# Optimization experiments

Measured on AMD Instinct MI355X. Metric: run time of the kernel, lower is better.

The kernel has to match this reference:

```python
import jax, jax.numpy as jnp
import numpy as np

B, L, D = 2, 2048, 2048
H, Hd = 16, 128


def _rotary_cos_sin(max_len, dim, base=10000.0):
    inv_freq = 1.0 / (base ** (np.arange(0, dim, 2, dtype=np.float32) / dim))
    t = np.arange(max_len, dtype=np.float32)
    freqs = np.outer(t, inv_freq)                      # [L, dim/2]
    emb = np.concatenate([freqs, freqs], axis=-1)      # [L, dim]
    cos = np.cos(emb)[None, None]                      # [1,1,L,dim]
    sin = np.sin(emb)[None, None]
    return jnp.asarray(cos), jnp.asarray(sin)


def setup_inputs() -> dict:
    key = jax.random.key(0)
    ks = jax.random.split(key, 5)
    hidden_states = jax.random.normal(ks[0], (B, L, D), dtype=jnp.float32)
    cos, sin = _rotary_cos_sin(L, Hd)
    s = 1.0 / np.sqrt(D)
    wq = jax.random.normal(ks[1], (H * Hd, D), dtype=jnp.float32) * s
    wk = jax.random.normal(ks[2], (H * Hd, D), dtype=jnp.float32) * s
    wv = jax.random.normal(ks[3], (H * Hd, D), dtype=jnp.float32) * s
    wo = jax.random.normal(ks[4], (D, H * Hd), dtype=jnp.float32) * s
    return {"hidden_states": hidden_states, "cos": cos, "sin": sin,
            "wq": wq, "wk": wk, "wv": wv, "wo": wo}


def _rotate_half(x):
    x1, x2 = jnp.split(x, 2, axis=-1)
    return jnp.concatenate([-x2, x1], axis=-1)


def reference(hidden_states, cos, sin, wq, wk, wv, wo):
    b, l, d = hidden_states.shape
    # QKV projections -> [B, H, L, Hd]
    q = (hidden_states @ wq.T).reshape(b, l, H, Hd).transpose(0, 2, 1, 3)
    k = (hidden_states @ wk.T).reshape(b, l, H, Hd).transpose(0, 2, 1, 3)
    v = (hidden_states @ wv.T).reshape(b, l, H, Hd).transpose(0, 2, 1, 3)
    c = cos[:, :, :l, :]
    s = sin[:, :, :l, :]
    q = q * c + _rotate_half(q) * s
    k = k * c + _rotate_half(k) * s
    # SDPA (non-causal, default scale = 1/sqrt(head_dim))
    scale = 1.0 / jnp.sqrt(jnp.asarray(Hd, dtype=q.dtype))
    scores = jnp.einsum('bhqd,bhkd->bhqk', q, k) * scale
    attn = jax.nn.softmax(scores, axis=-1)
    out = jnp.einsum('bhqk,bhkd->bhqd', attn, v)       # [B,H,L,Hd]
    out = out.transpose(0, 2, 1, 3).reshape(b, l, H * Hd)
    return out @ wo.T
```

## Files before the change

kernel.cpp:

```cpp
#include <hip/hip_runtime.h>

constexpr int Bb = 2;
constexpr int Ll = 2048;
constexpr int Dd = 2048;
constexpr int Hh = 16;
constexpr int Hd = 128;
constexpr int M  = Bb * Ll;

typedef __attribute__((ext_vector_type(8)))  short s16x8;
typedef __attribute__((ext_vector_type(4)))  float f32x4;
typedef __attribute__((ext_vector_type(16))) float f32x16;

__device__ __forceinline__ unsigned short f2bf(float f) {
    union { float f; unsigned u; } v; v.f = f;
    unsigned r = v.u + 0x7fffu + ((v.u >> 16) & 1u);
    return (unsigned short)(r >> 16);
}
__device__ __forceinline__ float bf2f(unsigned short b) {
    union { unsigned u; float f; } v; v.u = ((unsigned)b) << 16;
    return v.f;
}
__device__ __forceinline__ float fast_exp2(float x) {
#if __has_builtin(__builtin_amdgcn_exp2f)
    return __builtin_amdgcn_exp2f(x);
#else
    return exp2f(x);
#endif
}

__device__ __forceinline__ void gld16(const void* g, void* l) {
#if __has_builtin(__builtin_amdgcn_global_load_lds)
    __builtin_amdgcn_global_load_lds(
        (const __attribute__((address_space(1))) unsigned int*)g,
        (__attribute__((address_space(3))) unsigned int*)l, 16, 0, 0);
#else
    int lane = threadIdx.x & 63;
    ((int4*)l)[lane] = ((const int4*)g)[0];
#endif
}

__global__ __launch_bounds__(256)
void f2bf_kernel(const float* __restrict__ in, unsigned short* __restrict__ out, int n)
{
    int i = (blockIdx.x * 256 + threadIdx.x) * 4;
    if (i < n) {
        float4 v = *(const float4*)(in + i);
        ushort4 o;
        o.x = f2bf(v.x); o.y = f2bf(v.y); o.z = f2bf(v.z); o.w = f2bf(v.w);
        *(ushort4*)(out + i) = o;
    }
}

__global__ __launch_bounds__(512, 2)
void mfma_gemm_qkv(const unsigned short* __restrict__ A,
                   const unsigned short* __restrict__ Wall,
                   unsigned short* __restrict__ Oq,
                   unsigned short* __restrict__ Ok,
                   unsigned short* __restrict__ Ov)
{
    constexpr int K  = 2048;
    constexpr int NT = K / 64;
    constexpr int BM = 256, BN = 192;
    constexpr int SLOT_US = (BM + BN) * 64;

    __shared__ unsigned short lds[2 * SLOT_US];

    const int t    = threadIdx.x;
    const int w    = t >> 6, lane = t & 63;
    const int wm   = w >> 2, wn = w & 3;
    const int m0   = blockIdx.y * BM, n0 = blockIdx.x * BN;
    const int r16  = lane & 15, q4 = lane >> 4;
    const int lxor = (r16 & 7) << 4;

    const int srow8 = lane >> 3;
    const int sgcol = (((lane & 7) ^ srow8) << 4);
    const char* Agb = (const char*)A;
    const char* Wgb = (const char*)Wall;

    f32x4 acc[8][3];
#pragma unroll
    for (int i = 0; i < 8; ++i)
#pragma unroll
        for (int j = 0; j < 3; ++j)
            acc[i][j] = (f32x4){0.f, 0.f, 0.f, 0.f};

#define STAGE(tt, sl) do {                                                   \
    _Pragma("unroll") for (int p = 0; p < 4; ++p) {                          \
        int ia_ = w * 4 + p;                                                 \
        gld16(Agb + (size_t)(m0 + ia_ * 8 + srow8) * (K * 2) + (tt) * 128 + sgcol, \
              &lds[(sl) * SLOT_US + ia_ * 512]);                             \
    }                                                                        \
    _Pragma("unroll") for (int p = 0; p < 3; ++p) {                          \
        int ib_ = w * 3 + p;                                                 \
        gld16(Wgb + (size_t)(n0 + ib_ * 8 + srow8) * (K * 2) + (tt) * 128 + sgcol, \
              &lds[(sl) * SLOT_US + BM * 64 + ib_ * 512]);                   \
    }                                                                        \
} while (0)

    STAGE(0, 0);
    asm volatile("s_waitcnt vmcnt(0)" ::: "memory");
    __builtin_amdgcn_s_barrier();
    asm volatile("" ::: "memory");

    int slot = 0;
    for (int tt = 0; tt < NT; ++tt) {
        const char* Ab = (const char*)&lds[slot * SLOT_US];
        const char* Bp = (const char*)&lds[slot * SLOT_US + BM * 64];
        const int c0 = (q4 * 16) ^ lxor;
        const int c1 = (64 + q4 * 16) ^ lxor;

        s16x8 a0[8], a1[8], b0[3], b1[3];
#pragma unroll
        for (int mi = 0; mi < 8; ++mi) {
            int rb = (wm * 128 + mi * 16 + r16) * 128;
            a0[mi] = *(const s16x8*)(Ab + rb + c0);
        }
#pragma unroll
        for (int ni = 0; ni < 3; ++ni) {
            int rb = (wn * 48 + ni * 16 + r16) * 128;
            b0[ni] = *(const s16x8*)(Bp + rb + c0);
        }
        if (tt + 1 < NT) STAGE(tt + 1, slot ^ 1);
#pragma unroll
        for (int mi = 0; mi < 8; ++mi) {
            int rb = (wm * 128 + mi * 16 + r16) * 128;
            a1[mi] = *(const s16x8*)(Ab + rb + c1);
        }
#pragma unroll
        for (int ni = 0; ni < 3; ++ni) {
            int rb = (wn * 48 + ni * 16 + r16) * 128;
            b1[ni] = *(const s16x8*)(Bp + rb + c1);
        }

        __builtin_amdgcn_s_setprio(1);
#pragma unroll
        for (int mi = 0; mi < 8; ++mi)
#pragma unroll
            for (int ni = 0; ni < 3; ++ni)
                acc[mi][ni] = __builtin_amdgcn_mfma_f32_16x16x32_bf16(
                    a0[mi], b0[ni], acc[mi][ni], 0, 0, 0);
#pragma unroll
        for (int mi = 0; mi < 8; ++mi)
#pragma unroll
            for (int ni = 0; ni < 3; ++ni)
                acc[mi][ni] = __builtin_amdgcn_mfma_f32_16x16x32_bf16(
                    a1[mi], b1[ni], acc[mi][ni], 0, 0, 0);
        __builtin_amdgcn_s_setprio(0);

        asm volatile("s_waitcnt vmcnt(0)" ::: "memory");
        __builtin_amdgcn_s_barrier();
        asm volatile("" ::: "memory");
        slot ^= 1;
    }
#undef STAGE

#pragma unroll
    for (int ni = 0; ni < 3; ++ni) {
        int nb   = n0 + wn * 48 + ni * 16;
        int nsel = nb >> 11;
        int nr   = nb & 2047;
        int h    = nr >> 7;
        int d    = (nr & 127) + r16;
        if (nsel < 2) {
            unsigned short* O = nsel ? Ok : Oq;
#pragma unroll
            for (int mi = 0; mi < 8; ++mi)
#pragma unroll
                for (int r = 0; r < 4; ++r) {
                    int m = m0 + wm * 128 + mi * 16 + q4 * 4 + r;
                    int b = m >> 11, l = m & 2047;
                    O[(((size_t)b * Hh + h) * Ll + l) * Hd + d] =
                        f2bf(acc[mi][ni][r]);
                }
        } else {
#pragma unroll
            for (int mi = 0; mi < 8; ++mi) {
                int mb = m0 + wm * 128 + mi * 16 + q4 * 4;
                int b = mb >> 11, l = mb & 2047;
                ushort4 pk;
                pk.x = f2bf(acc[mi][ni][0]);
                pk.y = f2bf(acc[mi][ni][1]);
                pk.z = f2bf(acc[mi][ni][2]);
                pk.w = f2bf(acc[mi][ni][3]);
                *(ushort4*)&Ov[(((size_t)b * Hh + h) * Hd + d) * Ll + l] = pk;
            }
        }
    }
}

__global__ __launch_bounds__(512, 2)
void mfma_gemm_out(const unsigned short* __restrict__ A,
                   const unsigned short* __restrict__ W,
                   float* __restrict__ FO)
{
    constexpr int K  = 2048;
    constexpr int NT = K / 64;
    constexpr int SLOT_US = 24576;

    __shared__ unsigned short lds[3 * SLOT_US];

    const int t    = threadIdx.x;
    const int w    = t >> 6, lane = t & 63;
    const int wm   = w >> 1, wn = w & 1;
    const int m0   = blockIdx.y * 256, n0 = blockIdx.x * 128;
    const int r16  = lane & 15, q4 = lane >> 4;
    const int lxor = (r16 & 7) << 4;

    const int srow8 = lane >> 3;
    const int sgcol = (((lane & 7) ^ srow8) << 4);
    const char* Agb = (const char*)A;
    const char* Wgb = (const char*)W;

    f32x4 acc[4][4];
#pragma unroll
    for (int i = 0; i < 4; ++i)
#pragma unroll
        for (int j = 0; j < 4; ++j)
            acc[i][j] = (f32x4){0.f, 0.f, 0.f, 0.f};

    s16x8 af[4], bf[4];

#define STAGE_A(tt, sl, p) do {                                              \
    int ia_ = w * 4 + (p);                                                   \
    gld16(Agb + (size_t)(m0 + ia_ * 8 + srow8) * (K * 2) + (tt) * 128 + sgcol, \
          &lds[(sl) * SLOT_US + ia_ * 512]); } while (0)
#define STAGE_B(tt, sl, p) do {                                              \
    int ib_ = w * 2 + (p);                                                   \
    gld16(Wgb + (size_t)(n0 + ib_ * 8 + srow8) * (K * 2) + (tt) * 128 + sgcol, \
          &lds[(sl) * SLOT_US + 16384 + ib_ * 512]); } while (0)

#define LOAD_FRAGS(sl, ksub) do {                                            \
    const char* Ab_ = (const char*)&lds[(sl) * SLOT_US];                     \
    const char* Bb_ = (const char*)&lds[(sl) * SLOT_US + 16384];             \
    int cc_ = ((ksub) * 64 + q4 * 16) ^ lxor;                                \
    _Pragma("unroll") for (int mi = 0; mi < 4; ++mi)                         \
        af[mi] = *(const s16x8*)(Ab_ + (wm * 64 + mi * 16 + r16) * 128 + cc_); \
    _Pragma("unroll") for (int ni = 0; ni < 4; ++ni)                         \
        bf[ni] = *(const s16x8*)(Bb_ + (wn * 64 + ni * 16 + r16) * 128 + cc_); \
} while (0)

#define DO_MFMA() do {                                                       \
    __builtin_amdgcn_s_setprio(1);                                           \
    _Pragma("unroll") for (int mi = 0; mi < 4; ++mi)                         \
    _Pragma("unroll") for (int ni = 0; ni < 4; ++ni)                         \
        acc[mi][ni] = __builtin_amdgcn_mfma_f32_16x16x32_bf16(                \
            af[mi], bf[ni], acc[mi][ni], 0, 0, 0);                           \
    __builtin_amdgcn_s_setprio(0);                                           \
} while (0)

    STAGE_A(0, 0, 0); STAGE_A(0, 0, 1); STAGE_B(0, 0, 0);
    STAGE_A(0, 0, 2); STAGE_A(0, 0, 3); STAGE_B(0, 0, 1);
    STAGE_A(1, 1, 0); STAGE_A(1, 1, 1); STAGE_B(1, 1, 0);
    STAGE_A(1, 1, 2); STAGE_A(1, 1, 3); STAGE_B(1, 1, 1);
    asm volatile("s_waitcnt vmcnt(6)" ::: "memory");
    __builtin_amdgcn_s_barrier();
    asm volatile("" ::: "memory");

    int slot = 0;
    for (int tt = 0; tt < NT; ++tt) {
        int snx = slot + 2; if (snx >= 3) snx -= 3;
        const bool pf = (tt + 2 < NT);

        LOAD_FRAGS(slot, 0);
        if (pf) { STAGE_A(tt + 2, snx, 0); STAGE_A(tt + 2, snx, 1); STAGE_B(tt + 2, snx, 0); }
        asm volatile("" ::: "memory");
        __builtin_amdgcn_s_barrier();
        asm volatile("s_waitcnt lgkmcnt(0)" ::: "memory");
        DO_MFMA();
        asm volatile("" ::: "memory");
        __builtin_amdgcn_s_barrier();
        asm volatile("" ::: "memory");

        LOAD_FRAGS(slot, 1);
        if (pf) { STAGE_A(tt + 2, snx, 2); STAGE_A(tt + 2, snx, 3); STAGE_B(tt + 2, snx, 1); }
        asm volatile("" ::: "memory");
        __builtin_amdgcn_s_barrier();
        asm volatile("s_waitcnt lgkmcnt(0)" ::: "memory");
        DO_MFMA();
        if (pf)               asm volatile("s_waitcnt vmcnt(6)" ::: "memory");
        else if (tt + 1 < NT) asm volatile("s_waitcnt vmcnt(0)" ::: "memory");
        asm volatile("" ::: "memory");
        __builtin_amdgcn_s_barrier();
        asm volatile("" ::: "memory");

        slot = (slot == 2) ? 0 : slot + 1;
    }
#undef STAGE_A
#undef STAGE_B
#undef LOAD_FRAGS
#undef DO_MFMA

#pragma unroll
    for (int mi = 0; mi < 4; ++mi)
#pragma unroll
        for (int ni = 0; ni < 4; ++ni) {
            int n = n0 + wn * 64 + ni * 16 + r16;
#pragma unroll
            for (int r = 0; r < 4; ++r) {
                int m = m0 + wm * 64 + mi * 16 + q4 * 4 + r;
                FO[(size_t)m * Dd + n] = acc[mi][ni][r];
            }
        }
}

__global__ __launch_bounds__(256)
void rope_bf16(unsigned short* __restrict__ q, unsigned short* __restrict__ k,
               const float* __restrict__ cosb, const float* __restrict__ sinb)
{
    const float QS = 0.1275175f;
    const int t = threadIdx.x;
    int rblk = blockIdx.x;
    unsigned short* base;
    float sc;
    if (rblk < 4096) { base = q; sc = QS; }
    else             { base = k; sc = 1.0f; rblk -= 4096; }

    const int row = rblk * 16 + (t >> 4);
    const int l   = row & (Ll - 1);
    const int d0  = (t & 15) * 8;
    unsigned short* xr = base + (size_t)row * Hd;

    s16x8 v0 = *(const s16x8*)(xr + d0);
    s16x8 vp = *(const s16x8*)(xr + (d0 ^ 64));
    const float* cp = cosb + (size_t)l * Hd + d0;
    const float* sp = sinb + (size_t)l * Hd + d0;
    float4 c0 = *(const float4*)cp,       c1 = *(const float4*)(cp + 4);
    float4 sa = *(const float4*)sp,       sb = *(const float4*)(sp + 4);
    const float cc[8] = {c0.x, c0.y, c0.z, c0.w, c1.x, c1.y, c1.z, c1.w};
    const float ss[8] = {sa.x, sa.y, sa.z, sa.w, sb.x, sb.y, sb.z, sb.w};
    const float sgn = (d0 < 64) ? -1.f : 1.f;

    s16x8 o;
#pragma unroll
    for (int j = 0; j < 8; ++j) {
        float a = bf2f((unsigned short)v0[j]);
        float p = bf2f((unsigned short)vp[j]);
        float res = fmaf(a, cc[j], sgn * p * ss[j]) * sc;
        o[j] = (short)f2bf(res);
    }
    asm volatile("" ::: "memory");
    *(s16x8*)(xr + d0) = o;
}

__global__ __launch_bounds__(256)
void flash_attn(const unsigned short* __restrict__ q,
                const unsigned short* __restrict__ k,
                const unsigned short* __restrict__ vT,
                unsigned short* __restrict__ ctx)
{
    __shared__ unsigned short Ks[2][64 * 128];
    __shared__ unsigned short Vs[2][128 * 64];
    __shared__ unsigned short Ps[4][32 * 64];

    const int t = threadIdx.x;
    const int w = t >> 6, lane = t & 63;
    const int n32 = lane & 31, half = lane >> 5;
    const int bh = blockIdx.x >> 4;
    const int l0 = (blockIdx.x & 15) * 128;

    const unsigned short* qb = q  + ((size_t)bh * Ll + l0 + w * 32) * Hd;
    const unsigned short* kb = k  + (size_t)bh * Ll * Hd;
    const unsigned short* vb = vT + (size_t)bh * Hd * Ll;

    const int k_r = lane >> 4, k_u = lane & 15;
    const int v_r = lane >> 3, v_u = lane & 7;

#define STAGE(J0, bsel) do {                                                  \
    _Pragma("unroll") for (int p = 0; p < 4; ++p) {                           \
        int j_ = w * 4 + p;                                                   \
        int row_ = j_ * 4 + k_r;                                              \
        gld16(kb + (size_t)((J0) + row_) * Hd + ((k_u ^ (row_ & 7)) * 8),     \
              &Ks[bsel][j_ * 512]);                                           \
    }                                                                         \
    _Pragma("unroll") for (int p = 0; p < 4; ++p) {                           \
        int j_ = w * 4 + p;                                                   \
        int row_ = j_ * 8 + v_r;                                              \
        gld16(vb + (size_t)row_ * Ll + (J0) + ((v_u ^ (row_ & 7)) * 8),       \
              &Vs[bsel][j_ * 512]);                                           \
    }                                                                         \
} while (0)

    s16x8 qf[8];
#pragma unroll
    for (int ks = 0; ks < 8; ++ks)
        qf[ks] = *(const s16x8*)(qb + (size_t)n32 * Hd + ks * 16 + half * 8);

    f32x16 o[4];
    float lacc[16];
#pragma unroll
    for (int nt = 0; nt < 4; ++nt)
#pragma unroll
        for (int r = 0; r < 16; ++r) o[nt][r] = 0.f;
#pragma unroll
    for (int r = 0; r < 16; ++r) lacc[r] = 0.f;

    unsigned short* Pw = Ps[w];
    const int psw = (n32 & 7) << 3;

    STAGE(0, 0);
    __syncthreads();

    int buf = 0;
    for (int j0 = 0; j0 < Ll; j0 += 64) {
        if (j0 + 64 < Ll) STAGE(j0 + 64, buf ^ 1);

        f32x16 s0, s1;
#pragma unroll
        for (int r = 0; r < 16; ++r) { s0[r] = 0.f; s1[r] = 0.f; }
        __builtin_amdgcn_s_setprio(1);
#pragma unroll
        for (int ks = 0; ks < 8; ++ks) {
            int kc = (ks * 16 + half * 8) ^ psw;
            s16x8 b0 = *(const s16x8*)&Ks[buf][n32 * 128 + kc];
            s16x8 b1 = *(const s16x8*)&Ks[buf][(32 + n32) * 128 + kc];
            s0 = __builtin_amdgcn_mfma_f32_32x32x16_bf16(qf[ks], b0, s0, 0, 0, 0);
            s1 = __builtin_amdgcn_mfma_f32_32x32x16_bf16(qf[ks], b1, s1, 0, 0, 0);
        }
        __builtin_amdgcn_s_setprio(0);

#pragma unroll
        for (int r = 0; r < 16; ++r) {
            int mrow = (r & 3) + 8 * (r >> 2) + 4 * half;
            int sw = (mrow & 7) << 3;
            float p0 = fast_exp2(s0[r]);
            float p1 = fast_exp2(s1[r]);
            lacc[r] += p0 + p1;
            union { float f; unsigned u; } u0, u1;
            u0.f = p0; u1.f = p1;
            Pw[mrow * 64 + (n32 ^ sw)]        = (unsigned short)((u0.u + 0x8000u) >> 16);
            Pw[mrow * 64 + ((32 + n32) ^ sw)] = (unsigned short)((u1.u + 0x8000u) >> 16);
        }

        __builtin_amdgcn_s_setprio(1);
#pragma unroll
        for (int kst = 0; kst < 4; ++kst) {
            int cc = (kst * 16 + half * 8) ^ psw;
            s16x8 pf2 = *(const s16x8*)&Pw[n32 * 64 + cc];
#pragma unroll
            for (int nt = 0; nt < 4; ++nt) {
                s16x8 vf = *(const s16x8*)&Vs[buf][(nt * 32 + n32) * 64 + cc];
                o[nt] = __builtin_amdgcn_mfma_f32_32x32x16_bf16(pf2, vf, o[nt], 0, 0, 0);
            }
        }
        __builtin_amdgcn_s_setprio(0);

        __syncthreads();
        buf ^= 1;
    }
#undef STAGE

    float linv[16];
#pragma unroll
    for (int r = 0; r < 16; ++r) {
        float s = lacc[r];
        s += __shfl_xor(s, 1, 64);
        s += __shfl_xor(s, 2, 64);
        s += __shfl_xor(s, 4, 64);
        s += __shfl_xor(s, 8, 64);
        s += __shfl_xor(s, 16, 64);
        linv[r] = 1.0f / s;
    }

    const int b = bh >> 4, h = bh & 15;
#pragma unroll
    for (int nt = 0; nt < 4; ++nt)
#pragma unroll
        for (int r = 0; r < 16; ++r) {
            int mrow = (r & 3) + 8 * (r >> 2) + 4 * half;
            int lq = l0 + w * 32 + mrow;
            ctx[((size_t)(b * Ll + lq)) * Dd + h * Hd + nt * 32 + n32] =
                f2bf(o[nt][r] * linv[r]);
        }
}

extern "C" void kernel_launch(void* const* d_in, const int* in_sizes, int n_in,
                              void* d_out, int out_size, void* d_ws, size_t ws_size,
                              hipStream_t stream)
{
    const float* hs   = (const float*)d_in[0];
    const float* cosb = (const float*)d_in[1];
    const float* sinb = (const float*)d_in[2];
    const float* wq   = (const float*)d_in[3];
    const float* wk   = (const float*)d_in[4];
    const float* wv   = (const float*)d_in[5];
    const float* wo   = (const float*)d_in[6];
    float* out = (float*)d_out;

    char* ws = (char*)d_ws;
    unsigned short* Xb  = (unsigned short*)(ws);
    unsigned short* Wqb = (unsigned short*)(ws + (16ull << 20));
    unsigned short* Wkb = (unsigned short*)(ws + (24ull << 20));
    unsigned short* Wvb = (unsigned short*)(ws + (32ull << 20));
    unsigned short* Wob = (unsigned short*)(ws + (40ull << 20));
    unsigned short* qb  = (unsigned short*)(ws + (48ull << 20));
    unsigned short* kb  = (unsigned short*)(ws + (64ull << 20));
    unsigned short* vTb = (unsigned short*)(ws + (80ull << 20));
    unsigned short* ctx = Xb;

    const int nX = M * Dd;
    const int nW = Dd * Dd;

    f2bf_kernel<<<dim3(nX / 4 / 256), dim3(256), 0, stream>>>(hs, Xb, nX);
    f2bf_kernel<<<dim3(nW / 4 / 256), dim3(256), 0, stream>>>(wq, Wqb, nW);
    f2bf_kernel<<<dim3(nW / 4 / 256), dim3(256), 0, stream>>>(wk, Wkb, nW);
    f2bf_kernel<<<dim3(nW / 4 / 256), dim3(256), 0, stream>>>(wv, Wvb, nW);
    f2bf_kernel<<<dim3(nW / 4 / 256), dim3(256), 0, stream>>>(wo, Wob, nW);

    mfma_gemm_qkv<<<dim3(6144 / 192, M / 256), dim3(512), 0, stream>>>(
        Xb, Wqb, qb, kb, vTb);

    rope_bf16<<<dim3(2 * (Bb * Hh * Ll) / 16), dim3(256), 0, stream>>>(
        qb, kb, cosb, sinb);

    flash_attn<<<dim3(Bb * Hh * (Ll / 128)), dim3(256), 0, stream>>>(qb, kb, vTb, ctx);

    mfma_gemm_out<<<dim3(Dd / 128, M / 256), dim3(512), 0, stream>>>(
        ctx, Wob, out);
}
```

Baseline: 391.9 us.

## Split QKV GEMM k-step into four phases interleaving prefetch with MFMA

```diff
diff --git a/kernel.cpp b/kernel.cpp
--- a/kernel.cpp
+++ b/kernel.cpp
@@ -84,75 +84,93 @@
         for (int j = 0; j < 3; ++j)
             acc[i][j] = (f32x4){0.f, 0.f, 0.f, 0.f};
 
-#define STAGE(tt, sl) do {                                                   \
-    _Pragma("unroll") for (int p = 0; p < 4; ++p) {                          \
-        int ia_ = w * 4 + p;                                                 \
+#define STAGE_AF(tt, sl) do {                                                \
+    _Pragma("unroll") for (int p = 0; p < 2; ++p) {                          \
+        int ia_ = (w & 3) * 2 + (w >> 2) * 16 + p;                           \
         gld16(Agb + (size_t)(m0 + ia_ * 8 + srow8) * (K * 2) + (tt) * 128 + sgcol, \
               &lds[(sl) * SLOT_US + ia_ * 512]);                             \
-    }                                                                        \
+    } } while (0)
+#define STAGE_AS(tt, sl) do {                                                \
+    _Pragma("unroll") for (int p = 0; p < 2; ++p) {                          \
+        int ia_ = 8 + (w & 3) * 2 + (w >> 2) * 16 + p;                       \
+        gld16(Agb + (size_t)(m0 + ia_ * 8 + srow8) * (K * 2) + (tt) * 128 + sgcol, \
+              &lds[(sl) * SLOT_US + ia_ * 512]);                             \
+    } } while (0)
+#define STAGE_B(tt, sl) do {                                                 \
     _Pragma("unroll") for (int p = 0; p < 3; ++p) {                          \
         int ib_ = w * 3 + p;                                                 \
         gld16(Wgb + (size_t)(n0 + ib_ * 8 + srow8) * (K * 2) + (tt) * 128 + sgcol, \
               &lds[(sl) * SLOT_US + BM * 64 + ib_ * 512]);                   \
-    }                                                                        \
+    } } while (0)
+
+#define MFMA12(mbase) do {                                                   \
+    __builtin_amdgcn_s_setprio(1);                                           \
+    _Pragma("unroll") for (int mi = 0; mi < 4; ++mi)                         \
+    _Pragma("unroll") for (int ni = 0; ni < 3; ++ni)                         \
+        acc[(mbase) + mi][ni] = __builtin_amdgcn_mfma_f32_16x16x32_bf16(      \
+            a[mi], b[ni], acc[(mbase) + mi][ni], 0, 0, 0);                   \
+    __builtin_amdgcn_s_setprio(0);                                           \
 } while (0)
 
-    STAGE(0, 0);
+    STAGE_AF(0, 0); STAGE_B(0, 0); STAGE_AS(0, 0);
     asm volatile("s_waitcnt vmcnt(0)" ::: "memory");
     __builtin_amdgcn_s_barrier();
     asm volatile("" ::: "memory");
 
-    int slot = 0;
     for (int tt = 0; tt < NT; ++tt) {
+        const int slot = tt & 1, nsl = slot ^ 1;
+        const bool pf = (tt + 1 < NT);
         const char* Ab = (const char*)&lds[slot * SLOT_US];
         const char* Bp = (const char*)&lds[slot * SLOT_US + BM * 64];
         const int c0 = (q4 * 16) ^ lxor;
         const int c1 = (64 + q4 * 16) ^ lxor;
 
-        s16x8 a0[8], a1[8], b0[3], b1[3];
-#pragma unroll
-        for (int mi = 0; mi < 8; ++mi) {
-            int rb = (wm * 128 + mi * 16 + r16) * 128;
-            a0[mi] = *(const s16x8*)(Ab + rb + c0);
-        }
-#pragma unroll
-        for (int ni = 0; ni < 3; ++ni) {
-            int rb = (wn * 48 + ni * 16 + r16) * 128;
-            b0[ni] = *(const s16x8*)(Bp + rb + c0);
-        }
-        if (tt + 1 < NT) STAGE(tt + 1, slot ^ 1);
-#pragma unroll
-        for (int mi = 0; mi < 8; ++mi) {
-            int rb = (wm * 128 + mi * 16 + r16) * 128;
-            a1[mi] = *(const s16x8*)(Ab + rb + c1);
-        }
-#pragma unroll
-        for (int ni = 0; ni < 3; ++ni) {
-            int rb = (wn * 48 + ni * 16 + r16) * 128;
-            b1[ni] = *(const s16x8*)(Bp + rb + c1);
-        }
-
-        __builtin_amdgcn_s_setprio(1);
-#pragma unroll
-        for (int mi = 0; mi < 8; ++mi)
-#pragma unroll
-            for (int ni = 0; ni < 3; ++ni)
-                acc[mi][ni] = __builtin_amdgcn_mfma_f32_16x16x32_bf16(
-                    a0[mi], b0[ni], acc[mi][ni], 0, 0, 0);
-#pragma unroll
-        for (int mi = 0; mi < 8; ++mi)
-#pragma unroll
-            for (int ni = 0; ni < 3; ++ni)
-                acc[mi][ni] = __builtin_amdgcn_mfma_f32_16x16x32_bf16(
-                    a1[mi], b1[ni], acc[mi][ni], 0, 0, 0);
-        __builtin_amdgcn_s_setprio(0);
-
-        asm volatile("s_waitcnt vmcnt(0)" ::: "memory");
-        __builtin_amdgcn_s_barrier();
-        asm volatile("" ::: "memory");
-        slot ^= 1;
-    }
-#undef STAGE
+        s16x8 a[4], b[3];
+
+#pragma unroll
+        for (int mi = 0; mi < 4; ++mi)
+            a[mi] = *(const s16x8*)(Ab + (wm * 128 + mi * 16 + r16) * 128 + c0);
+#pragma unroll
+        for (int ni = 0; ni < 3; ++ni)
+            b[ni] = *(const s16x8*)(Bp + (wn * 48 + ni * 16 + r16) * 128 + c0);
+        if (pf) STAGE_AF(tt + 1, nsl);
+        MFMA12(0);
+        if (pf) asm volatile("s_waitcnt vmcnt(2)" ::: "memory");
+        else    asm volatile("s_waitcnt vmcnt(0)" ::: "memory");
+        __builtin_amdgcn_s_barrier();
+        asm volatile("" ::: "memory");
+
+#pragma unroll
+        for (int mi = 0; mi < 4; ++mi)
+            a[mi] = *(const s16x8*)(Ab + (wm * 128 + 64 + mi * 16 + r16) * 128 + c0);
+        if (pf) STAGE_B(tt + 1, nsl);
+        MFMA12(4);
+        __builtin_amdgcn_s_barrier();
+        asm volatile("" ::: "memory");
+
+#pragma unroll
+        for (int mi = 0; mi < 4; ++mi)
+            a[mi] = *(const s16x8*)(Ab + (wm * 128 + mi * 16 + r16) * 128 + c1);
+#pragma unroll
+        for (int ni = 0; ni < 3; ++ni)
+            b[ni] = *(const s16x8*)(Bp + (wn * 48 + ni * 16 + r16) * 128 + c1);
+        if (pf) STAGE_AS(tt + 1, nsl);
+        MFMA12(0);
+        __builtin_amdgcn_s_barrier();
+        asm volatile("" ::: "memory");
+
+#pragma unroll
+        for (int mi = 0; mi < 4; ++mi)
+            a[mi] = *(const s16x8*)(Ab + (wm * 128 + 64 + mi * 16 + r16) * 128 + c1);
+        MFMA12(4);
+        if (pf) asm volatile("s_waitcnt vmcnt(2)" ::: "memory");
+        __builtin_amdgcn_s_barrier();
+        asm volatile("" ::: "memory");
+    }
+#undef STAGE_AF
+#undef STAGE_AS
+#undef STAGE_B
+#undef MFMA12
 
 #pragma unroll
     for (int ni = 0; ni < 3; ++ni) {
```

Measured after the change: 402.6 us. 2.7% more time.

## Merge fp32-to-bf16 conversions into one launch and retile QKV GEMM to 128x192

Applied to the files above, without the earlier changes.

```diff
diff --git a/kernel.cpp b/kernel.cpp
--- a/kernel.cpp
+++ b/kernel.cpp
@@ -40,18 +40,28 @@
 }
 
 __global__ __launch_bounds__(256)
-void f2bf_kernel(const float* __restrict__ in, unsigned short* __restrict__ out, int n)
+void f2bf_all(const float* __restrict__ x,  const float* __restrict__ wq,
+              const float* __restrict__ wk, const float* __restrict__ wv,
+              const float* __restrict__ wo,
+              unsigned short* __restrict__ Xb,  unsigned short* __restrict__ Wqb,
+              unsigned short* __restrict__ Wkb, unsigned short* __restrict__ Wvb,
+              unsigned short* __restrict__ Wob)
 {
-    int i = (blockIdx.x * 256 + threadIdx.x) * 4;
-    if (i < n) {
-        float4 v = *(const float4*)(in + i);
-        ushort4 o;
-        o.x = f2bf(v.x); o.y = f2bf(v.y); o.z = f2bf(v.z); o.w = f2bf(v.w);
-        *(ushort4*)(out + i) = o;
-    }
-}
-
-__global__ __launch_bounds__(512, 2)
+    int bid = blockIdx.x;
+    const float* in; unsigned short* out; int off;
+    if      (bid <  8192) { in = x;  out = Xb;  off = bid; }
+    else if (bid < 12288) { in = wq; out = Wqb; off = bid - 8192; }
+    else if (bid < 16384) { in = wk; out = Wkb; off = bid - 12288; }
+    else if (bid < 20480) { in = wv; out = Wvb; off = bid - 16384; }
+    else                  { in = wo; out = Wob; off = bid - 20480; }
+    int i = (off * 256 + threadIdx.x) * 4;
+    float4 v = *(const float4*)(in + i);
+    ushort4 o;
+    o.x = f2bf(v.x); o.y = f2bf(v.y); o.z = f2bf(v.z); o.w = f2bf(v.w);
+    *(ushort4*)(out + i) = o;
+}
+
+__global__ __launch_bounds__(256, 2)
 void mfma_gemm_qkv(const unsigned short* __restrict__ A,
                    const unsigned short* __restrict__ Wall,
                    unsigned short* __restrict__ Oq,
@@ -60,14 +70,14 @@
 {
     constexpr int K  = 2048;
     constexpr int NT = K / 64;
-    constexpr int BM = 256, BN = 192;
+    constexpr int BM = 128, BN = 192;
     constexpr int SLOT_US = (BM + BN) * 64;
 
     __shared__ unsigned short lds[2 * SLOT_US];
 
     const int t    = threadIdx.x;
     const int w    = t >> 6, lane = t & 63;
-    const int wm   = w >> 2, wn = w & 3;
+    const int wm   = w >> 1, wn = w & 1;
     const int m0   = blockIdx.y * BM, n0 = blockIdx.x * BN;
     const int r16  = lane & 15, q4 = lane >> 4;
     const int lxor = (r16 & 7) << 4;
@@ -77,86 +87,76 @@
     const char* Agb = (const char*)A;
     const char* Wgb = (const char*)Wall;
 
-    f32x4 acc[8][3];
-#pragma unroll
-    for (int i = 0; i < 8; ++i)
-#pragma unroll
-        for (int j = 0; j < 3; ++j)
+    f32x4 acc[4][6];
+#pragma unroll
+    for (int i = 0; i < 4; ++i)
+#pragma unroll
+        for (int j = 0; j < 6; ++j)
             acc[i][j] = (f32x4){0.f, 0.f, 0.f, 0.f};
 
-#define STAGE(tt, sl) do {                                                   \
+#define STAGE_ALL(tt, sl) do {                                               \
     _Pragma("unroll") for (int p = 0; p < 4; ++p) {                          \
         int ia_ = w * 4 + p;                                                 \
         gld16(Agb + (size_t)(m0 + ia_ * 8 + srow8) * (K * 2) + (tt) * 128 + sgcol, \
               &lds[(sl) * SLOT_US + ia_ * 512]);                             \
     }                                                                        \
-    _Pragma("unroll") for (int p = 0; p < 3; ++p) {                          \
-        int ib_ = w * 3 + p;                                                 \
+    _Pragma("unroll") for (int p = 0; p < 6; ++p) {                          \
+        int ib_ = w * 6 + p;                                                 \
         gld16(Wgb + (size_t)(n0 + ib_ * 8 + srow8) * (K * 2) + (tt) * 128 + sgcol, \
               &lds[(sl) * SLOT_US + BM * 64 + ib_ * 512]);                   \
     }                                                                        \
 } while (0)
 
-    STAGE(0, 0);
+#define MFMA24() do {                                                        \
+    __builtin_amdgcn_s_setprio(1);                                           \
+    _Pragma("unroll") for (int mi = 0; mi < 4; ++mi)                         \
+    _Pragma("unroll") for (int ni = 0; ni < 6; ++ni)                         \
+        acc[mi][ni] = __builtin_amdgcn_mfma_f32_16x16x32_bf16(                \
+            a[mi], b[ni], acc[mi][ni], 0, 0, 0);                             \
+    __builtin_amdgcn_s_setprio(0);                                           \
+} while (0)
+
+    STAGE_ALL(0, 0);
     asm volatile("s_waitcnt vmcnt(0)" ::: "memory");
     __builtin_amdgcn_s_barrier();
     asm volatile("" ::: "memory");
 
-    int slot = 0;
     for (int tt = 0; tt < NT; ++tt) {
+        const int slot = tt & 1;
         const char* Ab = (const char*)&lds[slot * SLOT_US];
         const char* Bp = (const char*)&lds[slot * SLOT_US + BM * 64];
         const int c0 = (q4 * 16) ^ lxor;
         const int c1 = (64 + q4 * 16) ^ lxor;
 
-        s16x8 a0[8], a1[8], b0[3], b1[3];
-#pragma unroll
-        for (int mi = 0; mi < 8; ++mi) {
-            int rb = (wm * 128 + mi * 16 + r16) * 128;
-            a0[mi] = *(const s16x8*)(Ab + rb + c0);
-        }
-#pragma unroll
-        for (int ni = 0; ni < 3; ++ni) {
-            int rb = (wn * 48 + ni * 16 + r16) * 128;
-            b0[ni] = *(const s16x8*)(Bp + rb + c0);
-        }
-        if (tt + 1 < NT) STAGE(tt + 1, slot ^ 1);
-#pragma unroll
-        for (int mi = 0; mi < 8; ++mi) {
-            int rb = (wm * 128 + mi * 16 + r16) * 128;
-            a1[mi] = *(const s16x8*)(Ab + rb + c1);
-        }
-#pragma unroll
-        for (int ni = 0; ni < 3; ++ni) {
-            int rb = (wn * 48 + ni * 16 + r16) * 128;
-            b1[ni] = *(const s16x8*)(Bp + rb + c1);
-        }
-
-        __builtin_amdgcn_s_setprio(1);
-#pragma unroll
-        for (int mi = 0; mi < 8; ++mi)
-#pragma unroll
-            for (int ni = 0; ni < 3; ++ni)
-                acc[mi][ni] = __builtin_amdgcn_mfma_f32_16x16x32_bf16(
-                    a0[mi], b0[ni], acc[mi][ni], 0, 0, 0);
-#pragma unroll
-        for (int mi = 0; mi < 8; ++mi)
-#pragma unroll
-            for (int ni = 0; ni < 3; ++ni)
-                acc[mi][ni] = __builtin_amdgcn_mfma_f32_16x16x32_bf16(
-                    a1[mi], b1[ni], acc[mi][ni], 0, 0, 0);
-        __builtin_amdgcn_s_setprio(0);
+        s16x8 a[4], b[6];
+
+#pragma unroll
+        for (int mi = 0; mi < 4; ++mi)
+            a[mi] = *(const s16x8*)(Ab + (wm * 64 + mi * 16 + r16) * 128 + c0);
+#pragma unroll
+        for (int ni = 0; ni < 6; ++ni)
+            b[ni] = *(const s16x8*)(Bp + (wn * 96 + ni * 16 + r16) * 128 + c0);
+        if (tt + 1 < NT) STAGE_ALL(tt + 1, slot ^ 1);
+        MFMA24();
+
+#pragma unroll
+        for (int mi = 0; mi < 4; ++mi)
+            a[mi] = *(const s16x8*)(Ab + (wm * 64 + mi * 16 + r16) * 128 + c1);
+#pragma unroll
+        for (int ni = 0; ni < 6; ++ni)
+            b[ni] = *(const s16x8*)(Bp + (wn * 96 + ni * 16 + r16) * 128 + c1);
+        MFMA24();
 
         asm volatile("s_waitcnt vmcnt(0)" ::: "memory");
         __builtin_amdgcn_s_barrier();
         asm volatile("" ::: "memory");
-        slot ^= 1;
     }
-#undef STAGE
-
-#pragma unroll
-    for (int ni = 0; ni < 3; ++ni) {
-        int nb   = n0 + wn * 48 + ni * 16;
+#undef STAGE_ALL
+#undef MFMA24
+
+#pragma unroll
+    for (int ni = 0; ni < 6; ++ni) {
+        int nb   = n0 + wn * 96 + ni * 16;
         int nsel = nb >> 11;
         int nr   = nb & 2047;
         int h    = nr >> 7;
@@ -164,18 +164,18 @@
         if (nsel < 2) {
             unsigned short* O = nsel ? Ok : Oq;
 #pragma unroll
-            for (int mi = 0; mi < 8; ++mi)
+            for (int mi = 0; mi < 4; ++mi)
 #pragma unroll
                 for (int r = 0; r < 4; ++r) {
-                    int m = m0 + wm * 128 + mi * 16 + q4 * 4 + r;
+                    int m = m0 + wm * 64 + mi * 16 + q4 * 4 + r;
                     int b = m >> 11, l = m & 2047;
                     O[(((size_t)b * Hh + h) * Ll + l) * Hd + d] =
                         f2bf(acc[mi][ni][r]);
                 }
         } else {
 #pragma unroll
-            for (int mi = 0; mi < 8; ++mi) {
-                int mb = m0 + wm * 128 + mi * 16 + q4 * 4;
+            for (int mi = 0; mi < 4; ++mi) {
+                int mb = m0 + wm * 64 + mi * 16 + q4 * 4;
                 int b = mb >> 11, l = mb & 2047;
                 ushort4 pk;
                 pk.x = f2bf(acc[mi][ni][0]);
@@ -497,16 +497,10 @@
     unsigned short* vTb = (unsigned short*)(ws + (80ull << 20));
     unsigned short* ctx = Xb;
 
-    const int nX = M * Dd;
-    const int nW = Dd * Dd;
-
-    f2bf_kernel<<<dim3(nX / 4 / 256), dim3(256), 0, stream>>>(hs, Xb, nX);
-    f2bf_kernel<<<dim3(nW / 4 / 256), dim3(256), 0, stream>>>(wq, Wqb, nW);
-    f2bf_kernel<<<dim3(nW / 4 / 256), dim3(256), 0, stream>>>(wk, Wkb, nW);
-    f2bf_kernel<<<dim3(nW / 4 / 256), dim3(256), 0, stream>>>(wv, Wvb, nW);
-    f2bf_kernel<<<dim3(nW / 4 / 256), dim3(256), 0, stream>>>(wo, Wob, nW);
-
-    mfma_gemm_qkv<<<dim3(6144 / 192, M / 256), dim3(512), 0, stream>>>(
+    f2bf_all<<<dim3(24576), dim3(256), 0, stream>>>(
+        hs, wq, wk, wv, wo, Xb, Wqb, Wkb, Wvb, Wob);
+
+    mfma_gemm_qkv<<<dim3(6144 / 192, M / 128), dim3(256), 0, stream>>>(
         Xb, Wqb, qb, kb, vTb);
 
     rope_bf16<<<dim3(2 * (Bb * Hh * Ll) / 16), dim3(256), 0, stream>>>(
```

Result: no change. 386.2 us (-1.5%).
